# Kernel tuning notes

Measured on AMD Instinct MI355X. Metric: run time of the kernel, lower is better.

## Reference

```python
import jax, jax.numpy as jnp
import numpy as np

NUM_USERS = 100000
NUM_ITEMS = 50000
N_NODES = NUM_USERS + NUM_ITEMS
LATENT_DIM = 64
SBERT_DIM = 384
NUM_LAYERS = 3
N_EDGES = 2_000_000


def setup_inputs() -> dict:
    key = jax.random.key(0)
    k1, k2, k3, k4 = jax.random.split(key, 4)
    edge_index = jax.random.randint(k1, (2, N_EDGES), 0, N_NODES, dtype=jnp.int32)
    user_emb = jax.random.normal(k2, (NUM_USERS, LATENT_DIM), dtype=jnp.float32) * 0.1
    book_bert = jax.random.normal(k3, (NUM_ITEMS, SBERT_DIM), dtype=jnp.float32)
    # torch Linear weight layout: [out_features, in_features]
    w_proj = jax.random.normal(k4, (LATENT_DIM, SBERT_DIM), dtype=jnp.float32) * (1.0 / np.sqrt(SBERT_DIM))
    return {"edge_index": edge_index, "user_emb": user_emb, "book_bert": book_bert, "w_proj": w_proj}


def reference(edge_index, user_emb, book_bert, w_proj):
    src, dst = edge_index[0], edge_index[1]
    # initial embeddings: [users ; proj(book_bert)] -> [N, D]
    book_emb = book_bert @ w_proj.T
    emb0 = jnp.concatenate([user_emb, book_emb], axis=0)

    # symmetric gcn_norm without self-loops (PyG LGConv default)
    ones = jnp.ones((src.shape[0],), dtype=emb0.dtype)
    deg = jax.ops.segment_sum(ones, dst, num_segments=N_NODES)
    dis = jnp.where(deg > 0, jax.lax.rsqrt(jnp.maximum(deg, 1.0)), 0.0)
    norm = dis[src] * dis[dst]  # [E]

    x = emb0
    acc = emb0
    for _ in range(NUM_LAYERS):
        # out[dst] += norm * x[src]  (gather-scatter SpMM)
        msgs = norm[:, None] * x[src]  # [E, D]
        x = jax.ops.segment_sum(msgs, dst, num_segments=N_NODES)
        acc = acc + x
    out = acc / jnp.asarray(NUM_LAYERS + 1, dtype=emb0.dtype)
    return (emb0, out)
```

## Files before the change

### kernel.cpp

```cpp
#include <hip/hip_runtime.h>
#include <hip/hip_bf16.h>
#include <hip/hip_cooperative_groups.h>
#include <stdint.h>

namespace cg = cooperative_groups;

#define NUM_USERS 100000
#define NUM_ITEMS 50000
#define N_NODES   150000
#define LATENT    64
#define SBERT     384
#define N_EDGES   2000000
#define OUT_OFF   (N_NODES * LATENT)
#define NBUCK     586
#define BCAP      4096
#define EPB       4096
#define PBLK      2048
#define PWAVES    8192
#define NPW       19

typedef __hip_bfloat16 bf16;

__device__ __forceinline__ int ufl(int v) { return __builtin_amdgcn_readfirstlane(v); }

__device__ __forceinline__ unsigned short b16u(float f) {
    bf16 h = __float2bfloat16(f);
    return *reinterpret_cast<unsigned short*>(&h);
}

__global__ void k_zero_bcnt(int* __restrict__ bcnt) {
    int i = blockIdx.x * 256 + threadIdx.x;
    if (i < NBUCK) bcnt[i] = 0;
}

__global__ __launch_bounds__(256) void k_bin(const int* __restrict__ src,
                                             const int* __restrict__ dst,
                                             int* __restrict__ bcnt,
                                             unsigned* __restrict__ bin) {
    __shared__ int hist[NBUCK];
    __shared__ int base[NBUCK];
    const int tid = threadIdx.x;
    for (int i = tid; i < NBUCK; i += 256) hist[i] = 0;
    const int e0 = blockIdx.x * EPB;

    unsigned rec[16];
    int bb[16];
#pragma unroll
    for (int j = 0; j < 16; ++j) {
        int e = e0 + tid + j * 256;
        if (e < N_EDGES) {
            int d = __builtin_nontemporal_load(dst + e);
            int s = __builtin_nontemporal_load(src + e);
            bb[j]  = d >> 8;
            rec[j] = (unsigned)s | ((unsigned)(d & 255) << 18);
        } else {
            bb[j] = -1;
        }
    }
    __syncthreads();
#pragma unroll
    for (int j = 0; j < 16; ++j)
        if (bb[j] >= 0) atomicAdd(&hist[bb[j]], 1);
    __syncthreads();
    for (int i = tid; i < NBUCK; i += 256) {
        int c = hist[i];
        base[i] = c ? atomicAdd(&bcnt[i], c) : 0;
        hist[i] = 0;
    }
    __syncthreads();
    int p[16];
#pragma unroll
    for (int j = 0; j < 16; ++j)
        if (bb[j] >= 0) p[j] = atomicAdd(&hist[bb[j]], 1);
#pragma unroll
    for (int j = 0; j < 16; ++j)
        if (bb[j] >= 0)
            bin[(size_t)bb[j] * BCAP + base[bb[j]] + p[j]] = rec[j];
}

__global__ __launch_bounds__(1024) void k_bscan(const int* __restrict__ bcnt,
                                                int* __restrict__ bbase) {
    __shared__ int sm[1024];
    int tid = threadIdx.x;
    int v = (tid < NBUCK) ? bcnt[tid] : 0;
    sm[tid] = v;
    __syncthreads();
    for (int off = 1; off < 1024; off <<= 1) {
        int t = (tid >= off) ? sm[tid - off] : 0;
        __syncthreads();
        sm[tid] += t;
        __syncthreads();
    }
    if (tid <= NBUCK) bbase[tid] = (tid == 0) ? 0 : sm[tid - 1];
}

__global__ __launch_bounds__(256) void k_build(const unsigned* __restrict__ bin,
                                               const int* __restrict__ bcnt,
                                               const int* __restrict__ bbase,
                                               int* __restrict__ rp,
                                               float* __restrict__ dis,
                                               int* __restrict__ cws) {
    __shared__ int h[256];
    __shared__ int lc[256];
    const int tid   = threadIdx.x;
    const int b     = blockIdx.x;
    const int nbase = b << 8;
    const unsigned* mybin = bin + (size_t)b * BCAP;
    h[tid] = 0;
    __syncthreads();
    const int cnt  = bcnt[b];
    const int base = bbase[b];
    for (int i = tid; i < cnt; i += 256)
        atomicAdd(&h[__builtin_nontemporal_load(mybin + i) >> 18], 1);
    __syncthreads();
    int v = h[tid];
    __shared__ int sm[256];
    sm[tid] = v;
    __syncthreads();
    for (int off = 1; off < 256; off <<= 1) {
        int t = (tid >= off) ? sm[tid - off] : 0;
        __syncthreads();
        sm[tid] += t;
        __syncthreads();
    }
    int excl = sm[tid] - v;
    int n = nbase + tid;
    if (n < N_NODES) {
        rp[n]  = base + excl;
        dis[n] = (v > 0) ? rsqrtf((float)v) : 0.0f;
    }
    lc[tid] = base + excl;
    if (b == NBUCK - 1 && tid == 0) rp[N_NODES] = N_EDGES;
    __syncthreads();
    for (int i = tid; i < cnt; i += 256) {
        unsigned rec = __builtin_nontemporal_load(mybin + i);
        int dl = rec >> 18;
        int pos = atomicAdd(&lc[dl], 1);
        cws[pos] = (int)(rec & 0x3FFFF);
    }
}

__global__ void k_copy_user(const float4* __restrict__ u4, const float* __restrict__ dis,
                            float4* __restrict__ out4, uint2* __restrict__ y2) {
    int i = blockIdx.x * 256 + threadIdx.x;
    if (i < NUM_USERS * 16) {
        float4 v = u4[i];
        out4[i] = v;
        float d = dis[i >> 4];
        uint2 p;
        p.x = (unsigned)b16u(d * v.x) | ((unsigned)b16u(d * v.y) << 16);
        p.y = (unsigned)b16u(d * v.z) | ((unsigned)b16u(d * v.w) << 16);
        y2[i] = p;
    }
}

__global__ __launch_bounds__(256) void k_proj(const float* __restrict__ bert,
                                              const float* __restrict__ w,
                                              const float* __restrict__ dis,
                                              float* __restrict__ out,
                                              bf16* __restrict__ y) {
    __shared__ float sB[128][33];
    __shared__ float sW[32][64];
    const int tid  = threadIdx.x;
    const int rb   = blockIdx.x * 128;
    const int col8 = (tid & 7) * 8;
    const int rowg = (tid >> 3) * 4;

    float acc[4][8];
#pragma unroll
    for (int i = 0; i < 4; ++i)
#pragma unroll
        for (int j = 0; j < 8; ++j) acc[i][j] = 0.0f;

    for (int kb = 0; kb < SBERT; kb += 32) {
        __syncthreads();
#pragma unroll
        for (int j = 0; j < 4; ++j) {
            int idx = tid + j * 256;
            int r  = idx >> 3;
            int k4 = (idx & 7) * 4;
            int rr = min(rb + r, NUM_ITEMS - 1);
            const float* bp = bert + (size_t)rr * SBERT + kb + k4;
            float4 v = make_float4(__builtin_nontemporal_load(bp + 0),
                                   __builtin_nontemporal_load(bp + 1),
                                   __builtin_nontemporal_load(bp + 2),
                                   __builtin_nontemporal_load(bp + 3));
            sB[r][k4 + 0] = v.x; sB[r][k4 + 1] = v.y;
            sB[r][k4 + 2] = v.z; sB[r][k4 + 3] = v.w;
        }
#pragma unroll
        for (int j = 0; j < 2; ++j) {
            int idx = tid + j * 256;
            int c  = idx >> 3;
            int k4 = (idx & 7) * 4;
            float4 v = *(const float4*)(w + (size_t)c * SBERT + kb + k4);
            sW[k4 + 0][c] = v.x; sW[k4 + 1][c] = v.y;
            sW[k4 + 2][c] = v.z; sW[k4 + 3][c] = v.w;
        }
        __syncthreads();
#pragma unroll
        for (int kk = 0; kk < 32; ++kk) {
            float4 w0 = *(const float4*)&sW[kk][col8];
            float4 w1 = *(const float4*)&sW[kk][col8 + 4];
#pragma unroll
            for (int i = 0; i < 4; ++i) {
                float a = sB[rowg + i][kk];
                acc[i][0] = fmaf(a, w0.x, acc[i][0]);
                acc[i][1] = fmaf(a, w0.y, acc[i][1]);
                acc[i][2] = fmaf(a, w0.z, acc[i][2]);
                acc[i][3] = fmaf(a, w0.w, acc[i][3]);
                acc[i][4] = fmaf(a, w1.x, acc[i][4]);
                acc[i][5] = fmaf(a, w1.y, acc[i][5]);
                acc[i][6] = fmaf(a, w1.z, acc[i][6]);
                acc[i][7] = fmaf(a, w1.w, acc[i][7]);
            }
        }
    }
#pragma unroll
    for (int i = 0; i < 4; ++i) {
        int r = rb + rowg + i;
        if (r < NUM_ITEMS) {
            int n = NUM_USERS + r;
            size_t o = (size_t)n * LATENT + col8;
            float d = dis[n];
            float4 f0 = make_float4(acc[i][0], acc[i][1], acc[i][2], acc[i][3]);
            float4 f1 = make_float4(acc[i][4], acc[i][5], acc[i][6], acc[i][7]);
            *(float4*)(out + o)     = f0;
            *(float4*)(out + o + 4) = f1;
#pragma unroll
            for (int j = 0; j < 8; ++j) y[o + j] = __float2bfloat16(d * acc[i][j]);
        }
    }
}

__global__ __launch_bounds__(256, 8) void k_spmm3(const bf16* __restrict__ ye,
                                                  bf16* __restrict__ y0,
                                                  bf16* __restrict__ y1,
                                                  const int* __restrict__ rp,
                                                  const int* __restrict__ cws,
                                                  const float* __restrict__ dis,
                                                  float* __restrict__ out) {
    cg::grid_group grid = cg::this_grid();
    const int lane = threadIdx.x & 63;
    const int w    = ufl(blockIdx.x * 4 + (threadIdx.x >> 6));

    float acc[NPW];
#pragma unroll
    for (int k = 0; k < NPW; ++k) {
        int node = w + (k << 13);
        acc[k] = (node < N_NODES) ? out[(size_t)node * LATENT + lane] : 0.0f;
    }

    auto layer = [&](const bf16* __restrict__ ycur, bf16* __restrict__ ynext,
                     bool final_) {
#pragma unroll
        for (int k = 0; k < NPW; ++k) {
            int node = w + (k << 13);
            if (node < N_NODES) {
                int beg  = rp[node];
                int end  = rp[node + 1];
                int last = end - 1;
                float d  = dis[node];
                float a  = 0.0f;
                for (int base = beg; base < end; base += 16) {
                    int idx[16];
#pragma unroll
                    for (int j = 0; j < 16; ++j)
                        idx[j] = cws[min(base + j, last)];
                    float v[16];
#pragma unroll
                    for (int j = 0; j < 16; ++j)
                        v[j] = __bfloat162float(ycur[(size_t)idx[j] * LATENT + lane]);
#pragma unroll
                    for (int j = 0; j < 16; ++j)
                        if (base + j <= last) a += v[j];
                }
                acc[k] += d * a;
                if (!final_)
                    ynext[(size_t)node * LATENT + lane] = __float2bfloat16(d * d * a);
            }
        }
    };

    layer(ye, y0, false);
    grid.sync();
    layer(y0, y1, false);
    grid.sync();
    layer(y1, nullptr, true);

#pragma unroll
    for (int k = 0; k < NPW; ++k) {
        int node = w + (k << 13);
        if (node < N_NODES)
            out[OUT_OFF + (size_t)node * LATENT + lane] = acc[k] * 0.25f;
    }
}

template <bool FIRST, bool FINAL>
__global__ __launch_bounds__(256) void k_spmm(const bf16* __restrict__ y,
                                              const int* __restrict__ rp,
                                              const int* __restrict__ cws,
                                              const float* __restrict__ dis,
                                              bf16* __restrict__ yn,
                                              float* __restrict__ acc,
                                              const float* __restrict__ emb0) {
    int lane = threadIdx.x & 63;
    int node = ufl(blockIdx.x * 4 + (threadIdx.x >> 6));
    int beg = rp[node];
    int end = rp[node + 1];
    int last = end - 1;
    float d = dis[node];
    size_t o = (size_t)node * LATENT + lane;
    float accv = FIRST ? emb0[o] : acc[o];
    float a = 0.0f;
    for (int base = beg; base < end; base += 16) {
        int idx[16];
#pragma unroll
        for (int j = 0; j < 16; ++j)
            idx[j] = cws[min(base + j, last)];
        float v[16];
#pragma unroll
        for (int j = 0; j < 16; ++j)
            v[j] = __bfloat162float(y[(size_t)idx[j] * LATENT + lane]);
#pragma unroll
        for (int j = 0; j < 16; ++j)
            if (base + j <= last) a += v[j];
    }
    if (!FINAL) yn[o] = __float2bfloat16(d * d * a);
    float t = accv + d * a;
    acc[o] = FINAL ? t * 0.25f : t;
}

extern "C" void kernel_launch(void* const* d_in, const int* in_sizes, int n_in,
                              void* d_out, int out_size, void* d_ws, size_t ws_size,
                              hipStream_t stream) {
    const int*   ei    = (const int*)d_in[0];
    const float* uemb  = (const float*)d_in[1];
    const float* bert  = (const float*)d_in[2];
    const float* wproj = (const float*)d_in[3];
    float* out = (float*)d_out;

    char* ws = (char*)d_ws;
    size_t off = 0;
    auto carve = [&](size_t bytes) -> void* {
        void* p = ws + off;
        off += (bytes + 255) & ~(size_t)255;
        return p;
    };
    float*    dis    = (float*)carve(sizeof(float) * N_NODES);
    int*      rp     = (int*)carve(sizeof(int) * (N_NODES + 1));
    int*      bcnt   = (int*)carve(sizeof(int) * NBUCK);
    int*      bbase  = (int*)carve(sizeof(int) * (NBUCK + 1));
    unsigned* bin    = (unsigned*)carve(sizeof(unsigned) * (size_t)NBUCK * BCAP);
    int*      cws    = (int*)carve(sizeof(int) * N_EDGES);
    bf16*     ye     = (bf16*)carve(sizeof(bf16) * (size_t)N_NODES * LATENT);
    bf16*     y0     = (bf16*)carve(sizeof(bf16) * (size_t)N_NODES * LATENT);
    bf16*     y1     = (bf16*)carve(sizeof(bf16) * (size_t)N_NODES * LATENT);

    const int* srcI = ei;
    const int* dstI = ei + N_EDGES;

    k_zero_bcnt<<<(NBUCK + 255) / 256, 256, 0, stream>>>(bcnt);
    k_bin<<<(N_EDGES + EPB - 1) / EPB, 256, 0, stream>>>(srcI, dstI, bcnt, bin);
    k_bscan<<<1, 1024, 0, stream>>>(bcnt, bbase);
    k_build<<<NBUCK, 256, 0, stream>>>(bin, bcnt, bbase, rp, dis, cws);
    k_copy_user<<<(NUM_USERS * 16 + 255) / 256, 256, 0, stream>>>(
        (const float4*)uemb, dis, (float4*)out, (uint2*)ye);
    k_proj<<<(NUM_ITEMS + 127) / 128, 256, 0, stream>>>(bert, wproj, dis, out, ye);

    float* accp = out + OUT_OFF;

    static int coop_ok = -1;
    if (coop_ok < 0) {
        hipDeviceProp_t prop;
        int dev = 0;
        hipGetDevice(&dev);
        hipGetDeviceProperties(&prop, dev);
        int maxb = 0;
        hipError_t e = hipOccupancyMaxActiveBlocksPerMultiprocessor(
            &maxb, (const void*)k_spmm3, 256, 0);
        coop_ok = (e == hipSuccess && prop.cooperativeLaunch &&
                   maxb * prop.multiProcessorCount >= PBLK) ? 1 : 0;
    }

    if (coop_ok) {
        void* args[] = {(void*)&ye, (void*)&y0, (void*)&y1, (void*)&rp,
                        (void*)&cws, (void*)&dis, (void*)&out};
        hipLaunchCooperativeKernel((void*)k_spmm3, dim3(PBLK), dim3(256),
                                   args, 0, stream);
    } else {
        k_spmm<true,  false><<<N_NODES / 4, 256, 0, stream>>>(ye, rp, cws, dis, y0, accp, out);
        k_spmm<false, false><<<N_NODES / 4, 256, 0, stream>>>(y0, rp, cws, dis, y1, accp, out);
        k_spmm<false, true ><<<N_NODES / 4, 256, 0, stream>>>(y1, rp, cws, dis, y0, accp, out);
    }
}
```

Baseline: 434.5 us.

## Fuse whole pipeline into a single cooperative megakernel with grid syncs

Replaces the six preprocessing launches (zero, bin, scan, build, user copy, projection) plus the cooperative SpMM kernel with one persistent cooperative kernel of 1536 blocks. Phases are separated by grid.sync and share a union of shared-memory layouts. The aim is to remove per-launch overhead and inter-kernel gaps. In exchange, grid size drops from 2048 to 1536 blocks, occupancy is capped at 6 blocks per CU, each wave handles more nodes in the SpMM phase, and register pressure from the merged code may rise.

```diff
diff --git a/kernel.cpp b/kernel.cpp
--- a/kernel.cpp
+++ b/kernel.cpp
@@ -15,9 +15,12 @@
 #define NBUCK     586
 #define BCAP      4096
 #define EPB       4096
-#define PBLK      2048
-#define PWAVES    8192
-#define NPW       19
+
+#define NBM       1536
+#define EPBM      1303
+#define WAVESM    6144
+#define NPWM      25
+#define PROJ_TILES 391
 
 typedef __hip_bfloat16 bf16;
 
@@ -27,6 +30,7 @@
     bf16 h = __float2bfloat16(f);
     return *reinterpret_cast<unsigned short*>(&h);
 }
+
 
 __global__ void k_zero_bcnt(int* __restrict__ bcnt) {
     int i = blockIdx.x * 256 + threadIdx.x;
@@ -42,7 +46,6 @@
     const int tid = threadIdx.x;
     for (int i = tid; i < NBUCK; i += 256) hist[i] = 0;
     const int e0 = blockIdx.x * EPB;
-
     unsigned rec[16];
     int bb[16];
 #pragma unroll
@@ -53,9 +56,7 @@
             int s = __builtin_nontemporal_load(src + e);
             bb[j]  = d >> 8;
             rec[j] = (unsigned)s | ((unsigned)(d & 255) << 18);
-        } else {
-            bb[j] = -1;
-        }
+        } else bb[j] = -1;
     }
     __syncthreads();
 #pragma unroll
@@ -102,6 +103,7 @@
                                                int* __restrict__ cws) {
     __shared__ int h[256];
     __shared__ int lc[256];
+    __shared__ int sm[256];
     const int tid   = threadIdx.x;
     const int b     = blockIdx.x;
     const int nbase = b << 8;
@@ -114,7 +116,6 @@
         atomicAdd(&h[__builtin_nontemporal_load(mybin + i) >> 18], 1);
     __syncthreads();
     int v = h[tid];
-    __shared__ int sm[256];
     sm[tid] = v;
     __syncthreads();
     for (int off = 1; off < 256; off <<= 1) {
@@ -165,13 +166,11 @@
     const int rb   = blockIdx.x * 128;
     const int col8 = (tid & 7) * 8;
     const int rowg = (tid >> 3) * 4;
-
     float acc[4][8];
 #pragma unroll
     for (int i = 0; i < 4; ++i)
 #pragma unroll
         for (int j = 0; j < 8; ++j) acc[i][j] = 0.0f;
-
     for (int kb = 0; kb < SBERT; kb += 32) {
         __syncthreads();
 #pragma unroll
@@ -181,12 +180,10 @@
             int k4 = (idx & 7) * 4;
             int rr = min(rb + r, NUM_ITEMS - 1);
             const float* bp = bert + (size_t)rr * SBERT + kb + k4;
-            float4 v = make_float4(__builtin_nontemporal_load(bp + 0),
-                                   __builtin_nontemporal_load(bp + 1),
-                                   __builtin_nontemporal_load(bp + 2),
-                                   __builtin_nontemporal_load(bp + 3));
-            sB[r][k4 + 0] = v.x; sB[r][k4 + 1] = v.y;
-            sB[r][k4 + 2] = v.z; sB[r][k4 + 3] = v.w;
+            sB[r][k4 + 0] = __builtin_nontemporal_load(bp + 0);
+            sB[r][k4 + 1] = __builtin_nontemporal_load(bp + 1);
+            sB[r][k4 + 2] = __builtin_nontemporal_load(bp + 2);
+            sB[r][k4 + 3] = __builtin_nontemporal_load(bp + 3);
         }
 #pragma unroll
         for (int j = 0; j < 2; ++j) {
@@ -230,69 +227,6 @@
 #pragma unroll
             for (int j = 0; j < 8; ++j) y[o + j] = __float2bfloat16(d * acc[i][j]);
         }
-    }
-}
-
-__global__ __launch_bounds__(256, 8) void k_spmm3(const bf16* __restrict__ ye,
-                                                  bf16* __restrict__ y0,
-                                                  bf16* __restrict__ y1,
-                                                  const int* __restrict__ rp,
-                                                  const int* __restrict__ cws,
-                                                  const float* __restrict__ dis,
-                                                  float* __restrict__ out) {
-    cg::grid_group grid = cg::this_grid();
-    const int lane = threadIdx.x & 63;
-    const int w    = ufl(blockIdx.x * 4 + (threadIdx.x >> 6));
-
-    float acc[NPW];
-#pragma unroll
-    for (int k = 0; k < NPW; ++k) {
-        int node = w + (k << 13);
-        acc[k] = (node < N_NODES) ? out[(size_t)node * LATENT + lane] : 0.0f;
-    }
-
-    auto layer = [&](const bf16* __restrict__ ycur, bf16* __restrict__ ynext,
-                     bool final_) {
-#pragma unroll
-        for (int k = 0; k < NPW; ++k) {
-            int node = w + (k << 13);
-            if (node < N_NODES) {
-                int beg  = rp[node];
-                int end  = rp[node + 1];
-                int last = end - 1;
-                float d  = dis[node];
-                float a  = 0.0f;
-                for (int base = beg; base < end; base += 16) {
-                    int idx[16];
-#pragma unroll
-                    for (int j = 0; j < 16; ++j)
-                        idx[j] = cws[min(base + j, last)];
-                    float v[16];
-#pragma unroll
-                    for (int j = 0; j < 16; ++j)
-                        v[j] = __bfloat162float(ycur[(size_t)idx[j] * LATENT + lane]);
-#pragma unroll
-                    for (int j = 0; j < 16; ++j)
-                        if (base + j <= last) a += v[j];
-                }
-                acc[k] += d * a;
-                if (!final_)
-                    ynext[(size_t)node * LATENT + lane] = __float2bfloat16(d * d * a);
-            }
-        }
-    };
-
-    layer(ye, y0, false);
-    grid.sync();
-    layer(y0, y1, false);
-    grid.sync();
-    layer(y1, nullptr, true);
-
-#pragma unroll
-    for (int k = 0; k < NPW; ++k) {
-        int node = w + (k << 13);
-        if (node < N_NODES)
-            out[OUT_OFF + (size_t)node * LATENT + lane] = acc[k] * 0.25f;
     }
 }
 
@@ -331,6 +265,266 @@
     acc[o] = FINAL ? t * 0.25f : t;
 }
 
+
+struct SMbin   { int hist[NBUCK]; int base[NBUCK]; };
+struct SMscan  { int a[640]; int b[640]; };
+struct SMbuild { int h[256]; int lc[256]; int sm[256]; };
+struct SMproj  { float sB[128][33]; float sW[32][64]; };
+union  SMu { SMbin bin; SMscan scan; SMbuild build; SMproj proj; };
+
+__global__ __launch_bounds__(256, 6) void k_mega(const int* __restrict__ srcI,
+                                                 const int* __restrict__ dstI,
+                                                 const float* __restrict__ uemb,
+                                                 const float* __restrict__ bert,
+                                                 const float* __restrict__ wproj,
+                                                 int* __restrict__ bcnt,
+                                                 int* __restrict__ bbase,
+                                                 unsigned* __restrict__ bin,
+                                                 int* __restrict__ rp,
+                                                 float* __restrict__ dis,
+                                                 int* __restrict__ cws,
+                                                 bf16* __restrict__ ye,
+                                                 bf16* __restrict__ y0,
+                                                 bf16* __restrict__ y1,
+                                                 float* __restrict__ out) {
+    cg::grid_group grid = cg::this_grid();
+    __shared__ SMu smu;
+    const int tid = threadIdx.x;
+    const int bid = blockIdx.x;
+
+    {
+        int i = bid * 256 + tid;
+        if (i < NBUCK) bcnt[i] = 0;
+    }
+    grid.sync();
+
+    {
+        for (int i = tid; i < NBUCK; i += 256) smu.bin.hist[i] = 0;
+        const int e0 = bid * EPBM;
+        const int e1 = min(e0 + EPBM, N_EDGES);
+        unsigned rec[6];
+        int bb[6];
+#pragma unroll
+        for (int j = 0; j < 6; ++j) {
+            int e = e0 + tid + j * 256;
+            if (e < e1) {
+                int d = __builtin_nontemporal_load(dstI + e);
+                int s = __builtin_nontemporal_load(srcI + e);
+                bb[j]  = d >> 8;
+                rec[j] = (unsigned)s | ((unsigned)(d & 255) << 18);
+            } else bb[j] = -1;
+        }
+        __syncthreads();
+#pragma unroll
+        for (int j = 0; j < 6; ++j)
+            if (bb[j] >= 0) atomicAdd(&smu.bin.hist[bb[j]], 1);
+        __syncthreads();
+        for (int i = tid; i < NBUCK; i += 256) {
+            int c = smu.bin.hist[i];
+            smu.bin.base[i] = c ? atomicAdd(&bcnt[i], c) : 0;
+            smu.bin.hist[i] = 0;
+        }
+        __syncthreads();
+        int p[6];
+#pragma unroll
+        for (int j = 0; j < 6; ++j)
+            if (bb[j] >= 0) p[j] = atomicAdd(&smu.bin.hist[bb[j]], 1);
+#pragma unroll
+        for (int j = 0; j < 6; ++j)
+            if (bb[j] >= 0)
+                bin[(size_t)bb[j] * BCAP + smu.bin.base[bb[j]] + p[j]] = rec[j];
+    }
+    grid.sync();
+
+    if (bid == 0) {
+        int* A = smu.scan.a;
+        int* B = smu.scan.b;
+        for (int i = tid; i < NBUCK; i += 256) A[i] = bcnt[i];
+        __syncthreads();
+        for (int off = 1; off < NBUCK; off <<= 1) {
+            for (int i = tid; i < NBUCK; i += 256)
+                B[i] = (i >= off) ? A[i] + A[i - off] : A[i];
+            __syncthreads();
+            int* t = A; A = B; B = t;
+        }
+        for (int i = tid; i <= NBUCK; i += 256)
+            bbase[i] = (i == 0) ? 0 : A[i - 1];
+    }
+    grid.sync();
+
+    if (bid < NBUCK) {
+        const int nbase = bid << 8;
+        const unsigned* mybin = bin + (size_t)bid * BCAP;
+        smu.build.h[tid] = 0;
+        __syncthreads();
+        const int cnt  = bcnt[bid];
+        const int base = bbase[bid];
+        for (int i = tid; i < cnt; i += 256)
+            atomicAdd(&smu.build.h[__builtin_nontemporal_load(mybin + i) >> 18], 1);
+        __syncthreads();
+        int v = smu.build.h[tid];
+        smu.build.sm[tid] = v;
+        __syncthreads();
+        for (int off = 1; off < 256; off <<= 1) {
+            int t = (tid >= off) ? smu.build.sm[tid - off] : 0;
+            __syncthreads();
+            smu.build.sm[tid] += t;
+            __syncthreads();
+        }
+        int excl = smu.build.sm[tid] - v;
+        int n = nbase + tid;
+        if (n < N_NODES) {
+            rp[n]  = base + excl;
+            dis[n] = (v > 0) ? rsqrtf((float)v) : 0.0f;
+        }
+        smu.build.lc[tid] = base + excl;
+        if (bid == NBUCK - 1 && tid == 0) rp[N_NODES] = N_EDGES;
+        __syncthreads();
+        for (int i = tid; i < cnt; i += 256) {
+            unsigned rec = __builtin_nontemporal_load(mybin + i);
+            int dl = rec >> 18;
+            int pos = atomicAdd(&smu.build.lc[dl], 1);
+            cws[pos] = (int)(rec & 0x3FFFF);
+        }
+    }
+    grid.sync();
+
+    {
+        const float4* u4  = (const float4*)uemb;
+        float4* out4      = (float4*)out;
+        uint2* y2         = (uint2*)ye;
+        for (int i = bid * 256 + tid; i < NUM_USERS * 16; i += NBM * 256) {
+            float4 v = u4[i];
+            out4[i] = v;
+            float d = dis[i >> 4];
+            uint2 p;
+            p.x = (unsigned)b16u(d * v.x) | ((unsigned)b16u(d * v.y) << 16);
+            p.y = (unsigned)b16u(d * v.z) | ((unsigned)b16u(d * v.w) << 16);
+            y2[i] = p;
+        }
+    }
+    if (bid < PROJ_TILES) {
+        const int rb   = bid * 128;
+        const int col8 = (tid & 7) * 8;
+        const int rowg = (tid >> 3) * 4;
+        float acc[4][8];
+#pragma unroll
+        for (int i = 0; i < 4; ++i)
+#pragma unroll
+            for (int j = 0; j < 8; ++j) acc[i][j] = 0.0f;
+        for (int kb = 0; kb < SBERT; kb += 32) {
+            __syncthreads();
+#pragma unroll
+            for (int j = 0; j < 4; ++j) {
+                int idx = tid + j * 256;
+                int r  = idx >> 3;
+                int k4 = (idx & 7) * 4;
+                int rr = min(rb + r, NUM_ITEMS - 1);
+                const float* bp = bert + (size_t)rr * SBERT + kb + k4;
+                smu.proj.sB[r][k4 + 0] = __builtin_nontemporal_load(bp + 0);
+                smu.proj.sB[r][k4 + 1] = __builtin_nontemporal_load(bp + 1);
+                smu.proj.sB[r][k4 + 2] = __builtin_nontemporal_load(bp + 2);
+                smu.proj.sB[r][k4 + 3] = __builtin_nontemporal_load(bp + 3);
+            }
+#pragma unroll
+            for (int j = 0; j < 2; ++j) {
+                int idx = tid + j * 256;
+                int c  = idx >> 3;
+                int k4 = (idx & 7) * 4;
+                float4 v = *(const float4*)(wproj + (size_t)c * SBERT + kb + k4);
+                smu.proj.sW[k4 + 0][c] = v.x; smu.proj.sW[k4 + 1][c] = v.y;
+                smu.proj.sW[k4 + 2][c] = v.z; smu.proj.sW[k4 + 3][c] = v.w;
+            }
+            __syncthreads();
+#pragma unroll
+            for (int kk = 0; kk < 32; ++kk) {
+                float4 w0 = *(const float4*)&smu.proj.sW[kk][col8];
+                float4 w1 = *(const float4*)&smu.proj.sW[kk][col8 + 4];
+#pragma unroll
+                for (int i = 0; i < 4; ++i) {
+                    float a = smu.proj.sB[rowg + i][kk];
+                    acc[i][0] = fmaf(a, w0.x, acc[i][0]);
+                    acc[i][1] = fmaf(a, w0.y, acc[i][1]);
+                    acc[i][2] = fmaf(a, w0.z, acc[i][2]);
+                    acc[i][3] = fmaf(a, w0.w, acc[i][3]);
+                    acc[i][4] = fmaf(a, w1.x, acc[i][4]);
+                    acc[i][5] = fmaf(a, w1.y, acc[i][5]);
+                    acc[i][6] = fmaf(a, w1.z, acc[i][6]);
+                    acc[i][7] = fmaf(a, w1.w, acc[i][7]);
+                }
+            }
+        }
+#pragma unroll
+        for (int i = 0; i < 4; ++i) {
+            int r = rb + rowg + i;
+            if (r < NUM_ITEMS) {
+                int n = NUM_USERS + r;
+                size_t o = (size_t)n * LATENT + col8;
+                float d = dis[n];
+                float4 f0 = make_float4(acc[i][0], acc[i][1], acc[i][2], acc[i][3]);
+                float4 f1 = make_float4(acc[i][4], acc[i][5], acc[i][6], acc[i][7]);
+                *(float4*)(out + o)     = f0;
+                *(float4*)(out + o + 4) = f1;
+#pragma unroll
+                for (int j = 0; j < 8; ++j) ye[o + j] = __float2bfloat16(d * acc[i][j]);
+            }
+        }
+    }
+    grid.sync();
+
+    {
+        const int lane = tid & 63;
+        const int w    = ufl(bid * 4 + (tid >> 6));
+        float acc[NPWM];
+#pragma unroll
+        for (int k = 0; k < NPWM; ++k) {
+            int node = w + k * WAVESM;
+            acc[k] = (node < N_NODES) ? out[(size_t)node * LATENT + lane] : 0.0f;
+        }
+        auto layer = [&](const bf16* __restrict__ ycur, bf16* __restrict__ ynext,
+                         bool final_) {
+#pragma unroll
+            for (int k = 0; k < NPWM; ++k) {
+                int node = w + k * WAVESM;
+                if (node < N_NODES) {
+                    int beg  = rp[node];
+                    int end  = rp[node + 1];
+                    int last = end - 1;
+                    float d  = dis[node];
+                    float a  = 0.0f;
+                    for (int base = beg; base < end; base += 16) {
+                        int idx[16];
+#pragma unroll
+                        for (int j = 0; j < 16; ++j)
+                            idx[j] = cws[min(base + j, last)];
+                        float v[16];
+#pragma unroll
+                        for (int j = 0; j < 16; ++j)
+                            v[j] = __bfloat162float(ycur[(size_t)idx[j] * LATENT + lane]);
+#pragma unroll
+                        for (int j = 0; j < 16; ++j)
+                            if (base + j <= last) a += v[j];
+                    }
+                    acc[k] += d * a;
+                    if (!final_)
+                        ynext[(size_t)node * LATENT + lane] = __float2bfloat16(d * d * a);
+                }
+            }
+        };
+        layer(ye, y0, false);
+        grid.sync();
+        layer(y0, y1, false);
+        grid.sync();
+        layer(y1, nullptr, true);
+#pragma unroll
+        for (int k = 0; k < NPWM; ++k) {
+            int node = w + k * WAVESM;
+            if (node < N_NODES)
+                out[OUT_OFF + (size_t)node * LATENT + lane] = acc[k] * 0.25f;
+        }
+    }
+}
+
 extern "C" void kernel_launch(void* const* d_in, const int* in_sizes, int n_in,
                               void* d_out, int out_size, void* d_ws, size_t ws_size,
                               hipStream_t stream) {
@@ -360,16 +554,6 @@
     const int* srcI = ei;
     const int* dstI = ei + N_EDGES;
 
-    k_zero_bcnt<<<(NBUCK + 255) / 256, 256, 0, stream>>>(bcnt);
-    k_bin<<<(N_EDGES + EPB - 1) / EPB, 256, 0, stream>>>(srcI, dstI, bcnt, bin);
-    k_bscan<<<1, 1024, 0, stream>>>(bcnt, bbase);
-    k_build<<<NBUCK, 256, 0, stream>>>(bin, bcnt, bbase, rp, dis, cws);
-    k_copy_user<<<(NUM_USERS * 16 + 255) / 256, 256, 0, stream>>>(
-        (const float4*)uemb, dis, (float4*)out, (uint2*)ye);
-    k_proj<<<(NUM_ITEMS + 127) / 128, 256, 0, stream>>>(bert, wproj, dis, out, ye);
-
-    float* accp = out + OUT_OFF;
-
     static int coop_ok = -1;
     if (coop_ok < 0) {
         hipDeviceProp_t prop;
@@ -378,17 +562,27 @@
         hipGetDeviceProperties(&prop, dev);
         int maxb = 0;
         hipError_t e = hipOccupancyMaxActiveBlocksPerMultiprocessor(
-            &maxb, (const void*)k_spmm3, 256, 0);
+            &maxb, (const void*)k_mega, 256, 0);
         coop_ok = (e == hipSuccess && prop.cooperativeLaunch &&
-                   maxb * prop.multiProcessorCount >= PBLK) ? 1 : 0;
+                   maxb * prop.multiProcessorCount >= NBM) ? 1 : 0;
     }
 
     if (coop_ok) {
-        void* args[] = {(void*)&ye, (void*)&y0, (void*)&y1, (void*)&rp,
-                        (void*)&cws, (void*)&dis, (void*)&out};
-        hipLaunchCooperativeKernel((void*)k_spmm3, dim3(PBLK), dim3(256),
+        void* args[] = {(void*)&srcI, (void*)&dstI, (void*)&uemb, (void*)&bert,
+                        (void*)&wproj, (void*)&bcnt, (void*)&bbase, (void*)&bin,
+                        (void*)&rp, (void*)&dis, (void*)&cws, (void*)&ye,
+                        (void*)&y0, (void*)&y1, (void*)&out};
+        hipLaunchCooperativeKernel((void*)k_mega, dim3(NBM), dim3(256),
                                    args, 0, stream);
     } else {
+        k_zero_bcnt<<<(NBUCK + 255) / 256, 256, 0, stream>>>(bcnt);
+        k_bin<<<(N_EDGES + EPB - 1) / EPB, 256, 0, stream>>>(srcI, dstI, bcnt, bin);
+        k_bscan<<<1, 1024, 0, stream>>>(bcnt, bbase);
+        k_build<<<NBUCK, 256, 0, stream>>>(bin, bcnt, bbase, rp, dis, cws);
+        k_copy_user<<<(NUM_USERS * 16 + 255) / 256, 256, 0, stream>>>(
+            (const float4*)uemb, dis, (float4*)out, (uint2*)ye);
+        k_proj<<<(NUM_ITEMS + 127) / 128, 256, 0, stream>>>(bert, wproj, dis, out, ye);
+        float* accp = out + OUT_OFF;
         k_spmm<true,  false><<<N_NODES / 4, 256, 0, stream>>>(ye, rp, cws, dis, y0, accp, out);
         k_spmm<false, false><<<N_NODES / 4, 256, 0, stream>>>(y0, rp, cws, dis, y1, accp, out);
         k_spmm<false, true ><<<N_NODES / 4, 256, 0, stream>>>(y1, rp, cws, dis, y0, accp, out);
```

New measurement: 433.3 us. Within noise of the previous version (-0.3%).

## Replace bucketed CSR build with global-atomic degree count and three-pass scan

Applied to the files above, without the earlier changes.

Replaces the two-level bucket binning CSR construction (shared-memory histograms into bins, then a per-bucket local sort) with a plain global-atomic degree count, a three-kernel prefix scan, and an atomic-cursor scatter of source indices. It drops the bin staging buffer and its extra read/write pass, but adds global atomics on 150k counters and reads the edge list twice. It also switches the bert loads in the projection from scalar nontemporal loads to a plain float4 load. Edge order within each destination row becomes nondeterministic, which may change float summation order in the SpMM.

```diff
diff --git a/kernel.cpp b/kernel.cpp
--- a/kernel.cpp
+++ b/kernel.cpp
@@ -12,9 +12,8 @@
 #define SBERT     384
 #define N_EDGES   2000000
 #define OUT_OFF   (N_NODES * LATENT)
-#define NBUCK     586
-#define BCAP      4096
-#define EPB       4096
+#define CEB       4096
+#define SC1B      147
 #define PBLK      2048
 #define PWAVES    8192
 #define NPW       19
@@ -28,116 +27,98 @@
     return *reinterpret_cast<unsigned short*>(&h);
 }
 
-__global__ void k_zero_bcnt(int* __restrict__ bcnt) {
+__global__ void k_zero_deg(int* __restrict__ deg) {
     int i = blockIdx.x * 256 + threadIdx.x;
-    if (i < NBUCK) bcnt[i] = 0;
-}
-
-__global__ __launch_bounds__(256) void k_bin(const int* __restrict__ src,
-                                             const int* __restrict__ dst,
-                                             int* __restrict__ bcnt,
-                                             unsigned* __restrict__ bin) {
-    __shared__ int hist[NBUCK];
-    __shared__ int base[NBUCK];
-    const int tid = threadIdx.x;
-    for (int i = tid; i < NBUCK; i += 256) hist[i] = 0;
-    const int e0 = blockIdx.x * EPB;
-
-    unsigned rec[16];
-    int bb[16];
+    if (i < N_NODES) deg[i] = 0;
+}
+
+__global__ __launch_bounds__(256) void k_count(const int* __restrict__ dst,
+                                               int* __restrict__ deg) {
+    int e0 = blockIdx.x * CEB + threadIdx.x;
+    int d[16];
 #pragma unroll
     for (int j = 0; j < 16; ++j) {
-        int e = e0 + tid + j * 256;
-        if (e < N_EDGES) {
-            int d = __builtin_nontemporal_load(dst + e);
-            int s = __builtin_nontemporal_load(src + e);
-            bb[j]  = d >> 8;
-            rec[j] = (unsigned)s | ((unsigned)(d & 255) << 18);
-        } else {
-            bb[j] = -1;
-        }
-    }
-    __syncthreads();
+        int e = e0 + j * 256;
+        d[j] = (e < N_EDGES) ? __builtin_nontemporal_load(dst + e) : -1;
+    }
 #pragma unroll
     for (int j = 0; j < 16; ++j)
-        if (bb[j] >= 0) atomicAdd(&hist[bb[j]], 1);
-    __syncthreads();
-    for (int i = tid; i < NBUCK; i += 256) {
-        int c = hist[i];
-        base[i] = c ? atomicAdd(&bcnt[i], c) : 0;
-        hist[i] = 0;
-    }
-    __syncthreads();
-    int p[16];
-#pragma unroll
-    for (int j = 0; j < 16; ++j)
-        if (bb[j] >= 0) p[j] = atomicAdd(&hist[bb[j]], 1);
-#pragma unroll
-    for (int j = 0; j < 16; ++j)
-        if (bb[j] >= 0)
-            bin[(size_t)bb[j] * BCAP + base[bb[j]] + p[j]] = rec[j];
-}
-
-__global__ __launch_bounds__(1024) void k_bscan(const int* __restrict__ bcnt,
-                                                int* __restrict__ bbase) {
+        if (d[j] >= 0) atomicAdd(&deg[d[j]], 1);
+}
+
+__global__ __launch_bounds__(1024) void k_scan1(const int* __restrict__ deg,
+                                                int* __restrict__ rp,
+                                                int* __restrict__ bsum) {
     __shared__ int sm[1024];
-    int tid = threadIdx.x;
-    int v = (tid < NBUCK) ? bcnt[tid] : 0;
-    sm[tid] = v;
+    int t = threadIdx.x, b = blockIdx.x;
+    int i = b * 1024 + t;
+    int v = (i < N_NODES) ? deg[i] : 0;
+    sm[t] = v;
     __syncthreads();
     for (int off = 1; off < 1024; off <<= 1) {
-        int t = (tid >= off) ? sm[tid - off] : 0;
-        __syncthreads();
-        sm[tid] += t;
-        __syncthreads();
-    }
-    if (tid <= NBUCK) bbase[tid] = (tid == 0) ? 0 : sm[tid - 1];
-}
-
-__global__ __launch_bounds__(256) void k_build(const unsigned* __restrict__ bin,
-                                               const int* __restrict__ bcnt,
-                                               const int* __restrict__ bbase,
-                                               int* __restrict__ rp,
-                                               float* __restrict__ dis,
-                                               int* __restrict__ cws) {
-    __shared__ int h[256];
-    __shared__ int lc[256];
-    const int tid   = threadIdx.x;
-    const int b     = blockIdx.x;
-    const int nbase = b << 8;
-    const unsigned* mybin = bin + (size_t)b * BCAP;
-    h[tid] = 0;
-    __syncthreads();
-    const int cnt  = bcnt[b];
-    const int base = bbase[b];
-    for (int i = tid; i < cnt; i += 256)
-        atomicAdd(&h[__builtin_nontemporal_load(mybin + i) >> 18], 1);
-    __syncthreads();
-    int v = h[tid];
+        int x = (t >= off) ? sm[t - off] : 0;
+        __syncthreads();
+        sm[t] += x;
+        __syncthreads();
+    }
+    if (i < N_NODES) rp[i] = sm[t] - v;
+    if (t == 1023) bsum[b] = sm[1023];
+}
+
+__global__ __launch_bounds__(256) void k_scan2(const int* __restrict__ bsum,
+                                               int* __restrict__ bpre) {
     __shared__ int sm[256];
-    sm[tid] = v;
+    int t = threadIdx.x;
+    int v = (t < SC1B) ? bsum[t] : 0;
+    sm[t] = v;
     __syncthreads();
     for (int off = 1; off < 256; off <<= 1) {
-        int t = (tid >= off) ? sm[tid - off] : 0;
-        __syncthreads();
-        sm[tid] += t;
-        __syncthreads();
-    }
-    int excl = sm[tid] - v;
-    int n = nbase + tid;
-    if (n < N_NODES) {
-        rp[n]  = base + excl;
-        dis[n] = (v > 0) ? rsqrtf((float)v) : 0.0f;
-    }
-    lc[tid] = base + excl;
-    if (b == NBUCK - 1 && tid == 0) rp[N_NODES] = N_EDGES;
-    __syncthreads();
-    for (int i = tid; i < cnt; i += 256) {
-        unsigned rec = __builtin_nontemporal_load(mybin + i);
-        int dl = rec >> 18;
-        int pos = atomicAdd(&lc[dl], 1);
-        cws[pos] = (int)(rec & 0x3FFFF);
-    }
+        int x = (t >= off) ? sm[t - off] : 0;
+        __syncthreads();
+        sm[t] += x;
+        __syncthreads();
+    }
+    if (t < SC1B) bpre[t] = sm[t] - v;
+}
+
+__global__ __launch_bounds__(1024) void k_scan3(const int* __restrict__ deg,
+                                                int* __restrict__ rp,
+                                                int* __restrict__ cur,
+                                                float* __restrict__ dis,
+                                                const int* __restrict__ bpre) {
+    int t = threadIdx.x, b = blockIdx.x;
+    int i = b * 1024 + t;
+    if (i < N_NODES) {
+        int r = rp[i] + bpre[b];
+        rp[i]  = r;
+        cur[i] = r;
+        int dg = deg[i];
+        dis[i] = (dg > 0) ? rsqrtf((float)dg) : 0.0f;
+    }
+    if (i == 0) rp[N_NODES] = N_EDGES;
+}
+
+__global__ __launch_bounds__(256) void k_scatter(const int* __restrict__ src,
+                                                 const int* __restrict__ dst,
+                                                 int* __restrict__ cur,
+                                                 int* __restrict__ cws) {
+    int e0 = blockIdx.x * CEB + threadIdx.x;
+    int s[16], d[16];
+#pragma unroll
+    for (int j = 0; j < 16; ++j) {
+        int e = e0 + j * 256;
+        if (e < N_EDGES) {
+            d[j] = __builtin_nontemporal_load(dst + e);
+            s[j] = __builtin_nontemporal_load(src + e);
+        } else d[j] = -1;
+    }
+    int p[16];
+#pragma unroll
+    for (int j = 0; j < 16; ++j)
+        if (d[j] >= 0) p[j] = atomicAdd(&cur[d[j]], 1);
+#pragma unroll
+    for (int j = 0; j < 16; ++j)
+        if (d[j] >= 0) cws[p[j]] = s[j];
 }
 
 __global__ void k_copy_user(const float4* __restrict__ u4, const float* __restrict__ dis,
@@ -180,11 +161,7 @@
             int r  = idx >> 3;
             int k4 = (idx & 7) * 4;
             int rr = min(rb + r, NUM_ITEMS - 1);
-            const float* bp = bert + (size_t)rr * SBERT + kb + k4;
-            float4 v = make_float4(__builtin_nontemporal_load(bp + 0),
-                                   __builtin_nontemporal_load(bp + 1),
-                                   __builtin_nontemporal_load(bp + 2),
-                                   __builtin_nontemporal_load(bp + 3));
+            float4 v = *(const float4*)(bert + (size_t)rr * SBERT + kb + k4);
             sB[r][k4 + 0] = v.x; sB[r][k4 + 1] = v.y;
             sB[r][k4 + 2] = v.z; sB[r][k4 + 3] = v.w;
         }
@@ -347,23 +324,27 @@
         off += (bytes + 255) & ~(size_t)255;
         return p;
     };
-    float*    dis    = (float*)carve(sizeof(float) * N_NODES);
-    int*      rp     = (int*)carve(sizeof(int) * (N_NODES + 1));
-    int*      bcnt   = (int*)carve(sizeof(int) * NBUCK);
-    int*      bbase  = (int*)carve(sizeof(int) * (NBUCK + 1));
-    unsigned* bin    = (unsigned*)carve(sizeof(unsigned) * (size_t)NBUCK * BCAP);
-    int*      cws    = (int*)carve(sizeof(int) * N_EDGES);
-    bf16*     ye     = (bf16*)carve(sizeof(bf16) * (size_t)N_NODES * LATENT);
-    bf16*     y0     = (bf16*)carve(sizeof(bf16) * (size_t)N_NODES * LATENT);
-    bf16*     y1     = (bf16*)carve(sizeof(bf16) * (size_t)N_NODES * LATENT);
+    int*   deg  = (int*)carve(sizeof(int) * N_NODES);
+    int*   rp   = (int*)carve(sizeof(int) * (N_NODES + 1));
+    int*   cur  = (int*)carve(sizeof(int) * N_NODES);
+    float* dis  = (float*)carve(sizeof(float) * N_NODES);
+    int*   bsum = (int*)carve(sizeof(int) * SC1B);
+    int*   bpre = (int*)carve(sizeof(int) * SC1B);
+    int*   cws  = (int*)carve(sizeof(int) * N_EDGES);
+    bf16*  ye   = (bf16*)carve(sizeof(bf16) * (size_t)N_NODES * LATENT);
+    bf16*  y0   = (bf16*)carve(sizeof(bf16) * (size_t)N_NODES * LATENT);
+    bf16*  y1   = (bf16*)carve(sizeof(bf16) * (size_t)N_NODES * LATENT);
 
     const int* srcI = ei;
     const int* dstI = ei + N_EDGES;
 
-    k_zero_bcnt<<<(NBUCK + 255) / 256, 256, 0, stream>>>(bcnt);
-    k_bin<<<(N_EDGES + EPB - 1) / EPB, 256, 0, stream>>>(srcI, dstI, bcnt, bin);
-    k_bscan<<<1, 1024, 0, stream>>>(bcnt, bbase);
-    k_build<<<NBUCK, 256, 0, stream>>>(bin, bcnt, bbase, rp, dis, cws);
+    const int EB = (N_EDGES + CEB - 1) / CEB;
+    k_zero_deg<<<(N_NODES + 255) / 256, 256, 0, stream>>>(deg);
+    k_count<<<EB, 256, 0, stream>>>(dstI, deg);
+    k_scan1<<<SC1B, 1024, 0, stream>>>(deg, rp, bsum);
+    k_scan2<<<1, 256, 0, stream>>>(bsum, bpre);
+    k_scan3<<<SC1B, 1024, 0, stream>>>(deg, rp, cur, dis, bpre);
+    k_scatter<<<EB, 256, 0, stream>>>(srcI, dstI, cur, cws);
     k_copy_user<<<(NUM_USERS * 16 + 255) / 256, 256, 0, stream>>>(
         (const float4*)uemb, dis, (float4*)out, (uint2*)ye);
     k_proj<<<(NUM_ITEMS + 127) / 128, 256, 0, stream>>>(bert, wproj, dis, out, ye);
```

New measurement: 601.1 us. 1.38x slower.
